# Optimization experiments

Hardware: AMD Instinct MI355X
Metric: run time of the kernel (lower is better)

## Reference

```python
import jax, jax.numpy as jnp
import numpy as np
import math

SAMPLE_RATIO = 0.25
K = 5
EPS = 1e-6

def _cells(loc_orig, H, W):
    # map normalized [-1,1] coords to nearest grid cell index, as in tcformer token2map/map2token
    loc = jnp.clip(loc_orig, -1.0, 1.0)
    px = jnp.clip(jnp.round(0.5 * (loc[..., 0] + 1.0) * W - 0.5).astype(jnp.int32), 0, W - 1)
    py = jnp.clip(jnp.round(0.5 * (loc[..., 1] + 1.0) * H - 0.5).astype(jnp.int32), 0, H - 1)
    return py * W + px  # [B, N0]

def token2map(x, loc_orig, idx_agg, H, W):
    B, N, C = x.shape
    N0 = loc_orig.shape[1]
    cell = _cells(loc_orig, H, W)
    seg = (cell + jnp.arange(B)[:, None] * (H * W)).reshape(-1)
    feat = x[jnp.arange(B)[:, None], idx_agg]  # [B, N0, C] token feature per original point
    sums = jax.ops.segment_sum(feat.reshape(-1, C), seg, num_segments=B * H * W)
    cnt = jax.ops.segment_sum(jnp.ones((B * N0,), x.dtype), seg, num_segments=B * H * W)
    x_map = sums / (cnt[:, None] + EPS)  # per-cell mean over points hitting the cell
    return x_map.reshape(B, H, W, C).transpose(0, 3, 1, 2)

def map2token(x_map, N, loc_orig, idx_agg, agg_weight):
    B, C, H, W = x_map.shape
    cell = _cells(loc_orig, H, W)
    val = x_map.reshape(B, C, H * W).transpose(0, 2, 1)  # [B, HW, C]
    vpt = val[jnp.arange(B)[:, None], cell]              # [B, N0, C] map value at each point
    seg = (idx_agg + jnp.arange(B)[:, None] * N).reshape(-1)
    w = agg_weight.reshape(-1)
    wsum = jax.ops.segment_sum(w, seg, num_segments=B * N) + EPS
    ssum = jax.ops.segment_sum(vpt.reshape(-1, C) * w[:, None], seg, num_segments=B * N)
    return (ssum / wsum[:, None]).reshape(B, N, C)  # agg_weight-weighted mean per token

def token_cluster_merge(x, Ns, idx_agg, weight, k):
    B, N, C = x.shape
    # DPC-KNN clustering (index computation; mirrors torch.no_grad block)
    sq = jnp.sum(x * x, -1)
    d2 = jnp.clip(sq[:, :, None] + sq[:, None, :] - 2.0 * jnp.einsum('bnc,bmc->bnm', x, x), 0.0, None)
    dist = jnp.sqrt(d2) / (C ** 0.5)
    dnear = -jax.lax.top_k(-dist, k)[0]                  # k smallest distances (incl. self)
    density = jnp.exp(-jnp.mean(dnear * dnear, -1))
    mask = density[:, None, :] > density[:, :, None]
    dmax = jnp.max(dist.reshape(B, -1), -1)[:, None, None]
    parent_dist = jnp.min(jnp.where(mask, dist, dmax), -1)  # dist to nearest higher-density token
    score = parent_dist * density
    index_down = jax.lax.top_k(score, Ns)[1]             # [B, Ns] cluster centers
    idx_cluster = jnp.argmin(dist[jnp.arange(B)[:, None], index_down], axis=1)  # [B, N]
    idx_cluster = idx_cluster.at[jnp.arange(B)[:, None], index_down].set(jnp.arange(Ns)[None, :])
    # weighted merge of tokens into clusters
    seg = (idx_cluster + jnp.arange(B)[:, None] * Ns).reshape(-1)
    w = weight.reshape(-1)
    allw = jax.ops.segment_sum(w, seg, num_segments=B * Ns) + EPS
    norm_w = (w / allw[seg]).reshape(B, N)
    x_merged = jax.ops.segment_sum((x * norm_w[:, :, None]).reshape(-1, C), seg, num_segments=B * Ns).reshape(B, Ns, C)
    idx_agg_down = idx_cluster[jnp.arange(B)[:, None], idx_agg]      # compose index maps
    weight_t = norm_w[jnp.arange(B)[:, None], idx_agg][..., None]    # [B, N0, 1]
    return x_merged, idx_agg_down, weight_t

def _forward(x, loc_orig, idx_agg, agg_weight, idx_k_loc, H, W, conv_w, conv_b, skip_w, ln_g, ln_b, conf_w, conf_b):
    B, N, C = x.shape
    x_map = token2map(x, loc_orig, idx_agg, H, W)
    x_map = jax.lax.conv_general_dilated(x_map, conv_w, (2, 2), ((1, 1), (1, 1))) + conv_b[None, :, None, None]
    x_tok = map2token(x_map, N, loc_orig, idx_agg, agg_weight) + jnp.einsum('bnc,oc->bno', x, skip_w)
    mu = jnp.mean(x_tok, -1, keepdims=True)
    var = jnp.mean((x_tok - mu) ** 2, -1, keepdims=True)
    x_tok = (x_tok - mu) / jnp.sqrt(var + 1e-5) * ln_g + ln_b
    conf = jnp.einsum('bnc,oc->bno', x_tok, conf_w) + conf_b
    weight = jnp.exp(conf)
    Ns = max(math.ceil(N * SAMPLE_RATIO), 1)
    x_down, idx_agg_down, weight_t = token_cluster_merge(x_tok, Ns, idx_agg, weight, K)
    agg_weight_down = agg_weight * weight_t
    agg_weight_down = agg_weight_down / jnp.max(agg_weight_down, axis=1, keepdims=True)
    # down_block is an injected submodule; treated as identity passthrough here
    return x_down, idx_agg_down, agg_weight_down

def setup_inputs():
    key = jax.random.key(0)
    ks = jax.random.split(key, 8)
    B, N, C, N0, Cout = 8, 256, 256, 16384, 512
    return {
        'x': jax.random.normal(ks[0], (B, N, C), jnp.float32),
        'loc_orig': jax.random.uniform(ks[1], (B, N0, 2), jnp.float32, -1.0, 1.0),
        'idx_agg': jax.random.randint(ks[2], (B, N0), 0, N),
        'agg_weight': jax.random.uniform(ks[3], (B, N0, 1), jnp.float32, 0.1, 1.0),
        'idx_k_loc': jax.random.randint(ks[4], (B, N0, K), 0, N0),
        'H': 64, 'W': 64,
        'conv_w': jax.random.normal(ks[5], (Cout, C, 3, 3), jnp.float32) * 0.02,
        'conv_b': jnp.zeros((Cout,), jnp.float32),
        'skip_w': jax.random.normal(ks[6], (Cout, C), jnp.float32) * 0.02,
        'ln_g': jnp.ones((Cout,), jnp.float32),
        'ln_b': jnp.zeros((Cout,), jnp.float32),
        'conf_w': jax.random.normal(ks[7], (1, Cout), jnp.float32) * 0.02,
        'conf_b': jnp.zeros((1,), jnp.float32),
    }

def reference(x, loc_orig, idx_agg, agg_weight, idx_k_loc, H, W, conv_w, conv_b, skip_w, ln_g, ln_b, conf_w, conf_b):
    return _forward(x, loc_orig, idx_agg, agg_weight, idx_k_loc, H, W, conv_w, conv_b, skip_w, ln_g, ln_b, conf_w, conf_b)
```

## Files before the change

### kernel.cpp

```cpp
#include <hip/hip_runtime.h>
#include <math.h>

typedef unsigned long long ull;
typedef __attribute__((ext_vector_type(8))) short short8v;
typedef __attribute__((ext_vector_type(4))) float float4v;

#define NB   8
#define NTOK 256
#define CIN  256
#define NP   16384
#define NCO  512
#define HW64 4096
#define OHW  1024
#define NS   64
#define EPS  1e-6f
#define KC   2304
#define NKC  72

#define AS1 __attribute__((address_space(1)))
#define AS3 __attribute__((address_space(3)))
__device__ __forceinline__ void gl_lds16(const unsigned short* g, unsigned short* l) {
    __builtin_amdgcn_global_load_lds((const AS1 unsigned*)g, (AS3 unsigned*)l, 16, 0, 0);
}

constexpr size_t OFF_SUMS = 0;
constexpr size_t OFF_CNT  = OFF_SUMS + (size_t)NB*HW64*CIN;
constexpr size_t OFF_AMAT = OFF_CNT  + (size_t)NB*HW64;
constexpr size_t OFF_ALLW = OFF_AMAT + (size_t)NB*NTOK*OHW;
constexpr size_t OFF_DMAX = OFF_ALLW + (size_t)NB*NS;
constexpr size_t OFF_MAXW = OFF_DMAX + NB;
constexpr size_t OFF_ZG   = OFF_MAXW + NB;
constexpr size_t ZERO_END = OFF_ZG + 8;
constexpr size_t OFF_WT   = ZERO_END;
constexpr size_t OFF_SKWT = OFF_WT   + (size_t)KC*NCO;
constexpr size_t OFF_Y    = OFF_SKWT + (size_t)CIN*NCO;
constexpr size_t OFF_C2   = OFF_Y    + (size_t)NB*OHW*NCO;
constexpr size_t OFF_WSUM = OFF_C2   + (size_t)NB*NTOK*NCO;
constexpr size_t OFF_XSKIP= OFF_WSUM + (size_t)NB*NTOK;
constexpr size_t OFF_XTOK = OFF_XSKIP+ (size_t)NB*NTOK*NCO;
constexpr size_t OFF_XPK  = OFF_XTOK + (size_t)NB*NTOK*NCO;
constexpr size_t OFF_WEXP = OFF_XPK  + (size_t)NB*NTOK*NCO;
constexpr size_t OFF_SQ   = OFF_WEXP + (size_t)NB*NTOK;
constexpr size_t OFF_DIST = OFF_SQ   + (size_t)NB*NTOK;
constexpr size_t OFF_DENS = OFF_DIST + (size_t)NB*NTOK*NTOK;
constexpr size_t OFF_SCORE= OFF_DENS + (size_t)NB*NTOK;
constexpr size_t OFF_IND  = OFF_SCORE+ (size_t)NB*NTOK;
constexpr size_t OFF_IDXCL= OFF_IND  + (size_t)NB*NS;
constexpr size_t OFF_NORMW= OFF_IDXCL+ (size_t)NB*NTOK;
constexpr size_t OFF_AWBUF= OFF_NORMW+ (size_t)NB*NTOK;
constexpr size_t OFF_XTPK = OFF_AWBUF+ (size_t)NB*NP;
constexpr size_t OFF_AMATP2= OFF_XTPK + (size_t)NB*CIN*NTOK;
constexpr size_t OFF_XTOKPK= OFF_Y;

__device__ __forceinline__ unsigned pack_hl(float x) {
    unsigned u = __float_as_uint(x);
    unsigned t = u + 0x7fffu + ((u >> 16) & 1u);
    unsigned hibits = t & 0xffff0000u;
    float lo = x - __uint_as_float(hibits);
    unsigned ul = __float_as_uint(lo);
    unsigned lt = ul + 0x7fffu + ((ul >> 16) & 1u);
    return hibits | (lt >> 16);
}
__device__ __forceinline__ unsigned hp2(unsigned w0, unsigned w1) {
    return __builtin_amdgcn_perm(w1, w0, 0x07060302u);
}
__device__ __forceinline__ unsigned lp2(unsigned w0, unsigned w1) {
    return __builtin_amdgcn_perm(w1, w0, 0x05040100u);
}

__global__ void hist(const float* __restrict__ loc, const int* __restrict__ idxagg,
                     const float* __restrict__ aggw,
                     int* __restrict__ cntmat, float* __restrict__ cnt,
                     float* __restrict__ amat) {
    int bp = blockIdx.x*256 + threadIdx.x;
    int b  = bp >> 14;
    float lx = loc[2*bp+0], ly = loc[2*bp+1];
    lx = fminf(fmaxf(lx, -1.f), 1.f);
    ly = fminf(fmaxf(ly, -1.f), 1.f);
    int px = (int)rintf((lx + 1.f)*32.f - 0.5f); px = min(max(px,0),63);
    int py = (int)rintf((ly + 1.f)*32.f - 0.5f); py = min(max(py,0),63);
    int cell = py*64 + px;
    int tok = idxagg[bp];
    atomicAdd(&cntmat[((size_t)(b*HW64 + cell))*NTOK + tok], 1);
    atomicAdd(&cnt[b*HW64 + cell], 1.0f);
    int qx = (int)rintf((lx + 1.f)*16.f - 0.5f); qx = min(max(qx,0),31);
    int qy = (int)rintf((ly + 1.f)*16.f - 0.5f); qy = min(max(qy,0),31);
    atomicAdd(&amat[((size_t)(b*NTOK + tok))*OHW + qy*32 + qx], aggw[bp]);
}

__global__ void cnt_pack(unsigned* __restrict__ m) {
    size_t i = (size_t)blockIdx.x*256 + threadIdx.x;
    int4 v = ((const int4*)m)[i];
    uint4 o;
    o.x = pack_hl((float)v.x); o.y = pack_hl((float)v.y);
    o.z = pack_hl((float)v.z); o.w = pack_hl((float)v.w);
    ((uint4*)m)[i] = o;
}

__global__ void xt_pack(const float* __restrict__ x, unsigned* __restrict__ xtpk) {
    int id = blockIdx.x*256 + threadIdx.x;
    int tok = id & 255, cin = (id >> 8) & 255, b = id >> 16;
    xtpk[id] = pack_hl(x[((size_t)(b*NTOK + tok))*CIN + cin]);
}

__global__ void wtrans(const float* __restrict__ convw, uint4* __restrict__ wtf) {
    int tid = blockIdx.x*256 + threadIdx.x;
    int lane = tid & 63;
    int r1 = tid >> 6;
    int h = r1 & 1;
    int r2 = r1 >> 1;
    int f = r2 & 3;
    int r3 = r2 >> 2;
    int kc = r3 % NKC, mt = r3 / NKC;
    int cout = mt*64 + f*16 + (lane & 15);
    int kb = kc*32 + (lane >> 4)*8;
    unsigned s[8];
    #pragma unroll
    for (int j = 0; j < 8; ++j) {
        int k = kb + j;
        int grp = k >> 8, cin = k & 255;
        unsigned w = pack_hl(convw[(size_t)cout*KC + cin*9 + grp]);
        s[j] = h ? (w & 0xffffu) : (w >> 16);
    }
    uint4 o;
    o.x = s[0] | (s[1]<<16); o.y = s[2] | (s[3]<<16);
    o.z = s[4] | (s[5]<<16); o.w = s[6] | (s[7]<<16);
    wtf[tid] = o;
}

__global__ void pack4(const float4* __restrict__ src, uint4* __restrict__ dst) {
    size_t i = (size_t)blockIdx.x*256 + threadIdx.x;
    float4 v = src[i];
    uint4 o;
    o.x = pack_hl(v.x); o.y = pack_hl(v.y); o.z = pack_hl(v.z); o.w = pack_hl(v.w);
    dst[i] = o;
}

__launch_bounds__(512)
__global__ void map_gemm(const unsigned* __restrict__ A, const unsigned* __restrict__ B,
                         const float* __restrict__ cnt, unsigned short* __restrict__ planes) {
    __shared__ __align__(16) unsigned short Ah[4096];
    __shared__ __align__(16) unsigned short Bh[8192], Bl[8192];
    int z = blockIdx.z, m0 = blockIdx.y*128;
    const unsigned* Ab = A + ((size_t)z*HW64 + m0)*NTOK;
    const unsigned* Bb = B + (size_t)z*CIN*NTOK;
    int t = threadIdx.x, lane = t & 63;
    int w = t >> 6;
    int wm = w >> 2, wn = w & 3;
    int l15 = lane & 15, l4 = lane >> 4;
    int rowA = t & 127, kgA = t >> 7;
    int rowB = t & 255, kgB0 = (t >> 8)*2;
    const unsigned* arow = Ab + (size_t)rowA*NTOK + kgA*8;
    const unsigned* brow = Bb + (size_t)rowB*NTOK + kgB0*8;
    int wbA = (rowA>>4)*512 + kgA*128 + (rowA&15)*8;
    int wbB = (rowB>>4)*512 + kgB0*128 + (rowB&15)*8;

    float4v acc[4][4] = {};
    uint4 ra0, ra1, rb[2][2];
    auto loadA = [&](int kc) {
        const unsigned* p = arow + kc*32;
        ra0 = *(const uint4*)p; ra1 = *(const uint4*)(p + 4);
    };
    auto loadB = [&](int kc) {
        #pragma unroll
        for (int s = 0; s < 2; ++s) {
            const unsigned* p = brow + kc*32 + s*8;
            rb[s][0] = *(const uint4*)p; rb[s][1] = *(const uint4*)(p + 4);
        }
    };
    loadA(0); loadB(0);

    for (int kc = 0; kc < 8; ++kc) {
        __syncthreads();
        uint4 h, l;
        h.x=hp2(ra0.x,ra0.y); h.y=hp2(ra0.z,ra0.w); h.z=hp2(ra1.x,ra1.y); h.w=hp2(ra1.z,ra1.w);
        *(uint4*)&Ah[wbA] = h;
        #pragma unroll
        for (int s = 0; s < 2; ++s) {
            uint4 u0 = rb[s][0], u1 = rb[s][1];
            h.x=hp2(u0.x,u0.y); h.y=hp2(u0.z,u0.w); h.z=hp2(u1.x,u1.y); h.w=hp2(u1.z,u1.w);
            l.x=lp2(u0.x,u0.y); l.y=lp2(u0.z,u0.w); l.z=lp2(u1.x,u1.y); l.w=lp2(u1.z,u1.w);
            *(uint4*)&Bh[wbB + s*128] = h; *(uint4*)&Bl[wbB + s*128] = l;
        }
        __syncthreads();
        if (kc < 7) { loadA(kc+1); loadB(kc+1); }

        short8v bh[4], bl[4];
        #pragma unroll
        for (int q = 0; q < 4; ++q) {
            int off = (wn*4 + q)*512 + l4*128 + l15*8;
            bh[q] = *(const short8v*)&Bh[off];
            bl[q] = *(const short8v*)&Bl[off];
        }
        #pragma unroll
        for (int p = 0; p < 4; ++p) {
            int off = (wm*4 + p)*512 + l4*128 + l15*8;
            short8v ah = *(const short8v*)&Ah[off];
            #pragma unroll
            for (int q = 0; q < 4; ++q) {
                acc[p][q] = __builtin_amdgcn_mfma_f32_16x16x32_bf16(ah, bh[q], acc[p][q], 0, 0, 0);
                acc[p][q] = __builtin_amdgcn_mfma_f32_16x16x32_bf16(ah, bl[q], acc[p][q], 0, 0, 0);
            }
        }
    }

    const float* cntb = cnt + (size_t)z*HW64;
    #pragma unroll
    for (int p = 0; p < 4; ++p) {
        int mb = m0 + wm*64 + p*16 + l4*4;
        #pragma unroll
        for (int q = 0; q < 4; ++q) {
            int n = wn*64 + q*16 + l15;
            #pragma unroll
            for (int r = 0; r < 4; ++r) {
                float v = acc[p][q][r] / (cntb[mb + r] + EPS);
                unsigned pk = pack_hl(v);
                size_t grow = (size_t)z*HW64 + mb + r;
                size_t base = (grow >> 7)*65536 + (grow & 127)*256 + n;
                planes[base]         = (unsigned short)(pk >> 16);
                planes[base + 32768] = (unsigned short)(pk & 0xffffu);
            }
        }
    }
}

__launch_bounds__(256)
__global__ void conv_gemm(const unsigned short* __restrict__ planes,
                          const uint4* __restrict__ wtf,
                          const float* __restrict__ convb,
                          const unsigned short* __restrict__ zg,
                          unsigned* __restrict__ ytp) {
    __shared__ __align__(16) unsigned short AH[2][4096], AL[2][4096];
    int n0 = blockIdx.x * 128;
    int mt = blockIdx.y;
    int m0 = mt * 64;
    int t = threadIdx.x;
    int lane = t & 63, w = t >> 6;
    int wm = w >> 1, wn = w & 1;
    int l15 = lane & 15, l4 = lane >> 4;
    int kg = l4;

    int bbS[2], oyS[2], oxS[2];
    #pragma unroll
    for (int s = 0; s < 2; ++s) {
        int pos = n0 + (w + s*4)*16 + l15;
        bbS[s] = pos >> 10; int rem = pos & 1023;
        oyS[s] = rem >> 5; oxS[s] = rem & 31;
    }
    auto stage = [&](int kc, int buf) {
        int grp = kc >> 3;
        int ky = grp/3, kx = grp - 3*ky;
        int kin = (kc & 7)*32 + kg*8;
        #pragma unroll
        for (int s = 0; s < 2; ++s) {
            int iy = 2*oyS[s] - 1 + ky, ix = 2*oxS[s] - 1 + kx;
            bool ok = ((unsigned)iy < 64u) && ((unsigned)ix < 64u);
            int srow = bbS[s]*HW64 + iy*64 + ix;
            const unsigned short* sp = planes + ((size_t)(srow >> 7))*65536 + (srow & 127)*256 + kin;
            const unsigned short* ph = ok ? sp : zg;
            const unsigned short* pl = ok ? sp + 32768 : zg;
            gl_lds16(ph, &AH[buf][(w + s*4)*512]);
            gl_lds16(pl, &AL[buf][(w + s*4)*512]);
        }
    };

    const uint4* wbase = wtf + ((size_t)(((mt*NKC)*4 + wn*2)*2))*64 + lane;
    float4v acc[4][2] = {};
    short8v bhc[2], blc[2], bhn[2], bln[2];
    #pragma unroll
    for (int q = 0; q < 2; ++q) {
        bhc[q] = *(const short8v*)(wbase + q*128);
        blc[q] = *(const short8v*)(wbase + q*128 + 64);
    }
    stage(0, 0);
    __syncthreads();
    int cur = 0;

    for (int kc = 0; kc < NKC; ++kc) {
        bool nl = (kc + 1 < NKC);
        if (nl) {
            stage(kc+1, cur ^ 1);
            const uint4* wb = wbase + (size_t)(kc+1)*512;
            #pragma unroll
            for (int q = 0; q < 2; ++q) {
                bhn[q] = *(const short8v*)(wb + q*128);
                bln[q] = *(const short8v*)(wb + q*128 + 64);
            }
        }
        #pragma unroll
        for (int p = 0; p < 4; ++p) {
            int off = (wm*4 + p)*512 + l4*128 + l15*8;
            short8v ah = *(const short8v*)&AH[cur][off];
            short8v al = *(const short8v*)&AL[cur][off];
            #pragma unroll
            for (int q = 0; q < 2; ++q) {
                acc[p][q] = __builtin_amdgcn_mfma_f32_16x16x32_bf16(ah, bhc[q], acc[p][q], 0, 0, 0);
                acc[p][q] = __builtin_amdgcn_mfma_f32_16x16x32_bf16(ah, blc[q], acc[p][q], 0, 0, 0);
                acc[p][q] = __builtin_amdgcn_mfma_f32_16x16x32_bf16(al, bhc[q], acc[p][q], 0, 0, 0);
            }
        }
        if (nl) {
            #pragma unroll
            for (int q = 0; q < 2; ++q) { bhc[q] = bhn[q]; blc[q] = bln[q]; }
        }
        __syncthreads();
        cur ^= 1;
    }

    int bbk = n0 >> 10;
    int pos0 = (n0 & 1023) + wm*64;
    #pragma unroll
    for (int p = 0; p < 4; ++p) {
        int posb = pos0 + p*16 + l4*4;
        #pragma unroll
        for (int q = 0; q < 2; ++q) {
            int col = m0 + wn*32 + q*16 + l15;
            float bv = convb[col];
            uint4 o;
            o.x = pack_hl(acc[p][q][0] + bv);
            o.y = pack_hl(acc[p][q][1] + bv);
            o.z = pack_hl(acc[p][q][2] + bv);
            o.w = pack_hl(acc[p][q][3] + bv);
            *(uint4*)&ytp[((size_t)(bbk*NCO + col))*OHW + posb] = o;
        }
    }
}

template<int MODE, int TM, int TN>
__launch_bounds__(256)
__global__ void gemm_pk(const unsigned* __restrict__ A, const unsigned* __restrict__ B,
                        float* __restrict__ C, int K, int N,
                        long sA, long sB, long sC,
                        const float* __restrict__ aux, unsigned* __restrict__ dmaxU) {
    constexpr int NA = TM/64, NBs = TN/64;
    constexpr int WSM = TM/64;
    constexpr int WSN = 4/WSM;
    constexpr int TWM = TM/WSM, TWN = TN/WSN;
    constexpr int P = TWM/16, Q = TWN/16;
    __shared__ __align__(16) unsigned short Ahi[TM*32], Alo[TM*32];
    __shared__ __align__(16) unsigned short Bhi[TN*32], Blo[TN*32];
    int z = blockIdx.z;
    const unsigned* Ab = A + (size_t)z*sA;
    const unsigned* Bb = B + (size_t)z*sB;
    float* Cb = C + (size_t)z*sC;
    int n0 = blockIdx.x*TN, m0 = blockIdx.y*TM;
    int t = threadIdx.x;
    int lane = t & 63, wid = t >> 6;
    int wm = (WSM==2) ? (wid >> 1) : 0;
    int wn = (WSM==2) ? (wid & 1)  : wid;
    int l15 = lane & 15, l4 = lane >> 4;

    int rowA = t & (TM-1), kgA = t / TM;
    int rowB = t & (TN-1), kgB = t / TN;
    const unsigned* arow = Ab + (size_t)(m0 + rowA)*K + kgA*8;
    const unsigned* brw  = Bb + (size_t)(n0 + rowB)*K + kgB*8;
    int wbA = (rowA>>4)*512 + kgA*128 + (rowA&15)*8;
    int wbB = (rowB>>4)*512 + kgB*128 + (rowB&15)*8;

    float4v acc[P][Q] = {};
    uint4 ra[NA][2], rb[NBs][2];
    auto loadA = [&](int kc) {
        #pragma unroll
        for (int s = 0; s < NA; ++s) {
            const unsigned* p = arow + (size_t)kc*32 + s*16;
            ra[s][0] = *(const uint4*)p; ra[s][1] = *(const uint4*)(p + 4);
        }
    };
    auto loadB = [&](int kc) {
        #pragma unroll
        for (int s = 0; s < NBs; ++s) {
            const unsigned* p = brw + (size_t)kc*32 + s*16;
            rb[s][0] = *(const uint4*)p; rb[s][1] = *(const uint4*)(p + 4);
        }
    };
    loadA(0); loadB(0);
    int nkc = K >> 5;

    for (int kc = 0; kc < nkc; ++kc) {
        __syncthreads();
        uint4 h, l;
        #pragma unroll
        for (int s = 0; s < NA; ++s) {
            uint4 u0 = ra[s][0], u1 = ra[s][1];
            h.x=hp2(u0.x,u0.y); h.y=hp2(u0.z,u0.w); h.z=hp2(u1.x,u1.y); h.w=hp2(u1.z,u1.w);
            l.x=lp2(u0.x,u0.y); l.y=lp2(u0.z,u0.w); l.z=lp2(u1.x,u1.y); l.w=lp2(u1.z,u1.w);
            *(uint4*)&Ahi[wbA + s*256] = h; *(uint4*)&Alo[wbA + s*256] = l;
        }
        #pragma unroll
        for (int s = 0; s < NBs; ++s) {
            uint4 u0 = rb[s][0], u1 = rb[s][1];
            h.x=hp2(u0.x,u0.y); h.y=hp2(u0.z,u0.w); h.z=hp2(u1.x,u1.y); h.w=hp2(u1.z,u1.w);
            l.x=lp2(u0.x,u0.y); l.y=lp2(u0.z,u0.w); l.z=lp2(u1.x,u1.y); l.w=lp2(u1.z,u1.w);
            *(uint4*)&Bhi[wbB + s*256] = h; *(uint4*)&Blo[wbB + s*256] = l;
        }
        __syncthreads();
        if (kc + 1 < nkc) { loadA(kc+1); loadB(kc+1); }

        short8v bh[Q], bl[Q];
        #pragma unroll
        for (int q = 0; q < Q; ++q) {
            int off = (wn*Q + q)*512 + l4*128 + l15*8;
            bh[q] = *(const short8v*)&Bhi[off];
            bl[q] = *(const short8v*)&Blo[off];
        }
        #pragma unroll
        for (int p = 0; p < P; ++p) {
            int off = (wm*P + p)*512 + l4*128 + l15*8;
            short8v ah = *(const short8v*)&Ahi[off];
            short8v al = *(const short8v*)&Alo[off];
            #pragma unroll
            for (int q = 0; q < Q; ++q) {
                acc[p][q] = __builtin_amdgcn_mfma_f32_16x16x32_bf16(ah, bh[q], acc[p][q], 0, 0, 0);
                acc[p][q] = __builtin_amdgcn_mfma_f32_16x16x32_bf16(ah, bl[q], acc[p][q], 0, 0, 0);
                acc[p][q] = __builtin_amdgcn_mfma_f32_16x16x32_bf16(al, bh[q], acc[p][q], 0, 0, 0);
            }
        }
    }

    if (MODE == 0) {
        #pragma unroll
        for (int p = 0; p < P; ++p) {
            int mb = m0 + wm*TWM + p*16 + l4*4;
            #pragma unroll
            for (int q = 0; q < Q; ++q) {
                int n = n0 + wn*TWN + q*16 + l15;
                #pragma unroll
                for (int r = 0; r < 4; ++r)
                    Cb[(size_t)(mb + r)*N + n] = acc[p][q][r];
            }
        }
    } else {
        const float inv = 1.0f / sqrtf(512.0f);
        const float* sqb = aux + (size_t)z*NTOK;
        float tmax = 0.f;
        #pragma unroll
        for (int p = 0; p < P; ++p) {
            int mb = m0 + wm*TWM + p*16 + l4*4;
            #pragma unroll
            for (int q = 0; q < Q; ++q) {
                int n = n0 + wn*TWN + q*16 + l15;
                float sn = sqb[n];
                #pragma unroll
                for (int r = 0; r < 4; ++r) {
                    float d2 = sqb[mb + r] + sn - 2.0f*acc[p][q][r];
                    float d = sqrtf(fmaxf(d2, 0.0f)) * inv;
                    Cb[(size_t)(mb + r)*N + n] = d;
                    tmax = fmaxf(tmax, d);
                }
            }
        }
        __shared__ float redm[4];
        #pragma unroll
        for (int off = 32; off; off >>= 1) tmax = fmaxf(tmax, __shfl_xor(tmax, off, 64));
        if (lane == 0) redm[wid] = tmax;
        __syncthreads();
        if (t == 0) {
            float m = fmaxf(fmaxf(redm[0], redm[1]), fmaxf(redm[2], redm[3]));
            atomicMax(dmaxU + z, __float_as_uint(m));
        }
    }
}

__global__ void wsum_rows(const float* __restrict__ amat, float* __restrict__ wsum) {
    int row = blockIdx.x*4 + (threadIdx.x >> 6);
    int lane = threadIdx.x & 63;
    const float* ar = amat + (size_t)row*OHW;
    float s = 0.f;
    #pragma unroll
    for (int r = 0; r < 16; ++r) s += ar[lane + 64*r];
    #pragma unroll
    for (int off = 32; off; off >>= 1) s += __shfl_xor(s, off, 64);
    if (lane == 0) wsum[row] = s;
}

__device__ __forceinline__ float block_sum256(float v, float* red) {
    #pragma unroll
    for (int off = 32; off; off >>= 1) v += __shfl_xor(v, off, 64);
    __syncthreads();
    if ((threadIdx.x & 63) == 0) red[threadIdx.x >> 6] = v;
    __syncthreads();
    return red[0] + red[1] + red[2] + red[3];
}

__global__ void ln_conf(const float* __restrict__ C2, const float* __restrict__ wsum,
                        const float* __restrict__ xskip, const float* __restrict__ g,
                        const float* __restrict__ be, const float* __restrict__ confw,
                        const float* __restrict__ confb, float* __restrict__ xtok,
                        unsigned* __restrict__ xtokpk,
                        float* __restrict__ wexp, float* __restrict__ sqv) {
    __shared__ float red[4];
    int row = blockIdx.x, t = threadIdx.x;
    float ws = wsum[row] + EPS;
    size_t base = (size_t)row*NCO;
    float v0 = C2[base + t]       / ws + xskip[base + t];
    float v1 = C2[base + t + 256] / ws + xskip[base + t + 256];
    float mu  = block_sum256(v0 + v1, red) / 512.0f;
    float d0 = v0 - mu, d1 = v1 - mu;
    float var = block_sum256(d0*d0 + d1*d1, red) / 512.0f;
    float sv = sqrtf(var + 1e-5f);
    float x0 = d0/sv * g[t]       + be[t];
    float x1 = d1/sv * g[t + 256] + be[t + 256];
    xtok[base + t] = x0;
    xtok[base + t + 256] = x1;
    xtokpk[base + t] = pack_hl(x0);
    xtokpk[base + t + 256] = pack_hl(x1);
    float cs = block_sum256(x0*confw[t] + x1*confw[t + 256], red);
    float qs = block_sum256(x0*x0 + x1*x1, red);
    if (t == 0) {
        wexp[row] = expf(cs + confb[0]);
        sqv[row]  = qs;
    }
}

__global__ void knn_dens(const float* __restrict__ dist, float* __restrict__ dens) {
    int row = blockIdx.x*4 + (threadIdx.x >> 6);
    int lane = threadIdx.x & 63;
    const float* dr = dist + (size_t)row*NTOK;
    float v0 = dr[lane], v1 = dr[lane+64], v2 = dr[lane+128], v3 = dr[lane+192];
    float acc = 0.f;
    #pragma unroll
    for (int it = 0; it < 5; ++it) {
        float lm = fminf(fminf(v0, v1), fminf(v2, v3));
        float gm = lm;
        #pragma unroll
        for (int off = 32; off; off >>= 1) gm = fminf(gm, __shfl_xor(gm, off, 64));
        acc += gm*gm;
        ull ball = __ballot(lm == gm);
        int first = __ffsll(ball) - 1;
        if (lane == first) {
            if      (v0 == gm) v0 = 1e30f;
            else if (v1 == gm) v1 = 1e30f;
            else if (v2 == gm) v2 = 1e30f;
            else               v3 = 1e30f;
        }
    }
    if (lane == 0) dens[row] = expf(-(acc/5.0f));
}

__global__ void parent_score(const float* __restrict__ dist, const float* __restrict__ dens,
                             const unsigned* __restrict__ dmaxU, float* __restrict__ score) {
    int row = blockIdx.x*4 + (threadIdx.x >> 6);
    int lane = threadIdx.x & 63;
    int b = row >> 8;
    float di = dens[row];
    float dm = __uint_as_float(dmaxU[b]);
    const float* dr = dist + (size_t)row*NTOK;
    const float* db = dens + (size_t)b*NTOK;
    float pd = dm;
    #pragma unroll
    for (int r = 0; r < 4; ++r) {
        int j = lane + 64*r;
        pd = fminf(pd, (db[j] > di) ? dr[j] : dm);
    }
    #pragma unroll
    for (int off = 32; off; off >>= 1) pd = fminf(pd, __shfl_xor(pd, off, 64));
    if (lane == 0) score[row] = pd * di;
}

__global__ void topk64(const float* __restrict__ score, int* __restrict__ ind) {
    int b = blockIdx.x, lane = threadIdx.x;
    const float* sb = score + b*NTOK;
    ull k0, k1, k2, k3;
    {
        unsigned i0 = lane, i1 = lane+64, i2 = lane+128, i3 = lane+192;
        k0 = ((ull)(__float_as_uint(sb[i0]) + 1u) << 32) | (unsigned)(4095 - i0);
        k1 = ((ull)(__float_as_uint(sb[i1]) + 1u) << 32) | (unsigned)(4095 - i1);
        k2 = ((ull)(__float_as_uint(sb[i2]) + 1u) << 32) | (unsigned)(4095 - i2);
        k3 = ((ull)(__float_as_uint(sb[i3]) + 1u) << 32) | (unsigned)(4095 - i3);
    }
    for (int it = 0; it < 64; ++it) {
        ull lm = k0;
        if (k1 > lm) lm = k1;
        if (k2 > lm) lm = k2;
        if (k3 > lm) lm = k3;
        ull gm = lm;
        #pragma unroll
        for (int off = 32; off; off >>= 1) {
            ull o = __shfl_xor(gm, off, 64);
            if (o > gm) gm = o;
        }
        if (lane == 0) ind[b*NS + it] = 4095 - (int)(gm & 0xffffffffull);
        if      (k0 == gm) k0 = 0;
        else if (k1 == gm) k1 = 0;
        else if (k2 == gm) k2 = 0;
        else if (k3 == gm) k3 = 0;
    }
}

__global__ void assign_k(const float* __restrict__ dist, const int* __restrict__ ind,
                         int* __restrict__ idxcl) {
    int row = blockIdx.x*4 + (threadIdx.x >> 6);
    int lane = threadIdx.x & 63;
    int b = row >> 8, i = row & 255;
    int center = ind[b*NS + lane];
    float d = dist[((size_t)(b*NTOK + center))*NTOK + i];
    ull key = ((ull)__float_as_uint(d) << 32) | (unsigned)lane;
    #pragma unroll
    for (int off = 32; off; off >>= 1) {
        ull o = __shfl_xor(key, off, 64);
        if (o < key) key = o;
    }
    if (lane == 0) idxcl[row] = (int)(key & 0xffffffffull);
}

__global__ void center_set(const int* __restrict__ ind, int* __restrict__ idxcl) {
    int id = threadIdx.x;
    int b = id >> 6, s = id & 63;
    idxcl[b*NTOK + ind[id]] = s;
}

__global__ void allw_acc(const int* __restrict__ idxcl, const float* __restrict__ wexp,
                         float* __restrict__ allw) {
    int b = blockIdx.x, i = threadIdx.x;
    atomicAdd(&allw[b*NS + idxcl[b*NTOK + i]], wexp[b*NTOK + i]);
}

__global__ void normw_k(const int* __restrict__ idxcl, const float* __restrict__ wexp,
                        const float* __restrict__ allw, float* __restrict__ normw) {
    int b = blockIdx.x, i = threadIdx.x;
    normw[b*NTOK + i] = wexp[b*NTOK + i] / (allw[b*NS + idxcl[b*NTOK + i]] + EPS);
}

__global__ void merge_k(const float* __restrict__ xtok, const int* __restrict__ idxcl,
                        const float* __restrict__ normw, float* __restrict__ xout) {
    int row = blockIdx.x, t = threadIdx.x;
    int b = row >> 8;
    int cl = idxcl[row];
    float nw = normw[row];
    float* o = xout + ((size_t)(b*NS + cl))*NCO;
    const float* xr = xtok + (size_t)row*NCO;
    atomicAdd(&o[t],       xr[t]       * nw);
    atomicAdd(&o[t + 256], xr[t + 256] * nw);
}

__global__ void out_idx_aw(const int* __restrict__ idxagg, const float* __restrict__ aggw,
                           const int* __restrict__ idxcl, const float* __restrict__ normw,
                           float* __restrict__ dout, float* __restrict__ awbuf,
                           unsigned* __restrict__ maxw) {
    __shared__ float red[4];
    int bp = blockIdx.x*256 + threadIdx.x;
    int b = bp >> 14;
    int tok = idxagg[bp];
    int cl = idxcl[b*NTOK + tok];
    dout[(size_t)NB*NS*NCO + bp] = (float)cl;
    float aw = aggw[bp] * normw[b*NTOK + tok];
    awbuf[bp] = aw;
    float m = aw;
    #pragma unroll
    for (int off = 32; off; off >>= 1) m = fmaxf(m, __shfl_xor(m, off, 64));
    if ((threadIdx.x & 63) == 0) red[threadIdx.x >> 6] = m;
    __syncthreads();
    if (threadIdx.x == 0) {
        float mm = fmaxf(fmaxf(red[0], red[1]), fmaxf(red[2], red[3]));
        atomicMax(&maxw[b], __float_as_uint(mm));
    }
}

__global__ void aw_final(const float* __restrict__ awbuf, const float* __restrict__ maxw,
                         float* __restrict__ dout) {
    int bp = blockIdx.x*256 + threadIdx.x;
    int b = bp >> 14;
    dout[(size_t)NB*NS*NCO + (size_t)NB*NP + bp] = awbuf[bp] / maxw[b];
}

extern "C" void kernel_launch(void* const* d_in, const int* in_sizes, int n_in,
                              void* d_out, int out_size, void* d_ws, size_t ws_size,
                              hipStream_t stream) {
    const float* x      = (const float*)d_in[0];
    const float* loc    = (const float*)d_in[1];
    const int*   idxagg = (const int*)  d_in[2];
    const float* aggw   = (const float*)d_in[3];
    const float* convw  = (const float*)d_in[7];
    const float* convb  = (const float*)d_in[8];
    const float* skipw  = (const float*)d_in[9];
    const float* lng    = (const float*)d_in[10];
    const float* lnb    = (const float*)d_in[11];
    const float* confw  = (const float*)d_in[12];
    const float* confb  = (const float*)d_in[13];

    float* ws = (float*)d_ws;
    float* dout = (float*)d_out;

    (void)hipMemsetAsync(ws, 0, ZERO_END*sizeof(float), stream);
    (void)hipMemsetAsync(dout, 0, (size_t)NB*NS*NCO*sizeof(float), stream);

    hist<<<dim3(NB*NP/256), 256, 0, stream>>>(loc, idxagg, aggw,
                                              (int*)(ws + OFF_SUMS), ws + OFF_CNT, ws + OFF_AMAT);
    cnt_pack<<<dim3(NB*HW64*CIN/1024), 256, 0, stream>>>((unsigned*)(ws + OFF_SUMS));
    xt_pack<<<dim3(NB*CIN*NTOK/256), 256, 0, stream>>>(x, (unsigned*)(ws + OFF_XTPK));
    wtrans<<<dim3(1152), 256, 0, stream>>>(convw, (uint4*)(ws + OFF_WT));
    pack4<<<dim3(CIN*NCO/1024), 256, 0, stream>>>((const float4*)skipw, (uint4*)(ws + OFF_SKWT));
    pack4<<<dim3(NB*NTOK*CIN/1024), 256, 0, stream>>>((const float4*)x, (uint4*)(ws + OFF_XPK));

    map_gemm<<<dim3(1, 32, 8), 512, 0, stream>>>((const unsigned*)(ws + OFF_SUMS),
                                                 (const unsigned*)(ws + OFF_XTPK),
                                                 ws + OFF_CNT,
                                                 (unsigned short*)(ws + OFF_SUMS));

    conv_gemm<<<dim3(64, 8), 256, 0, stream>>>((const unsigned short*)(ws + OFF_SUMS),
                                               (const uint4*)(ws + OFF_WT), convb,
                                               (const unsigned short*)(ws + OFF_ZG),
                                               (unsigned*)(ws + OFF_Y));

    wsum_rows<<<dim3(NB*NTOK/4), 256, 0, stream>>>(ws + OFF_AMAT, ws + OFF_WSUM);
    pack4<<<dim3(NB*NTOK*OHW/1024), 256, 0, stream>>>((const float4*)(ws + OFF_AMAT),
                                                      (uint4*)(ws + OFF_AMATP2));
    gemm_pk<0,64,64><<<dim3(8, 4, 8), 256, 0, stream>>>((const unsigned*)(ws + OFF_AMATP2),
                                                  (const unsigned*)(ws + OFF_Y),
                                                  ws + OFF_C2, OHW, NCO,
                                                  (long)NTOK*OHW, (long)NCO*OHW, (long)NTOK*NCO,
                                                  nullptr, nullptr);
    gemm_pk<0,64,64><<<dim3(8, 32, 1), 256, 0, stream>>>((const unsigned*)(ws + OFF_XPK),
                                                   (const unsigned*)(ws + OFF_SKWT),
                                                   ws + OFF_XSKIP, CIN, NCO, 0, 0, 0,
                                                   nullptr, nullptr);

    ln_conf<<<dim3(NB*NTOK), 256, 0, stream>>>(ws + OFF_C2, ws + OFF_WSUM, ws + OFF_XSKIP,
                                               lng, lnb, confw, confb,
                                               ws + OFF_XTOK, (unsigned*)(ws + OFF_XTOKPK),
                                               ws + OFF_WEXP, ws + OFF_SQ);

    gemm_pk<1,64,64><<<dim3(4, 4, 8), 256, 0, stream>>>((const unsigned*)(ws + OFF_XTOKPK),
                                                  (const unsigned*)(ws + OFF_XTOKPK),
                                                  ws + OFF_DIST, NCO, NTOK,
                                                  (long)NTOK*NCO, (long)NTOK*NCO, (long)NTOK*NTOK,
                                                  ws + OFF_SQ, (unsigned*)(ws + OFF_DMAX));

    knn_dens<<<dim3(NB*NTOK/4), 256, 0, stream>>>(ws + OFF_DIST, ws + OFF_DENS);
    parent_score<<<dim3(NB*NTOK/4), 256, 0, stream>>>(ws + OFF_DIST, ws + OFF_DENS,
                                                      (const unsigned*)(ws + OFF_DMAX), ws + OFF_SCORE);
    topk64<<<dim3(NB), 64, 0, stream>>>(ws + OFF_SCORE, (int*)(ws + OFF_IND));
    assign_k<<<dim3(NB*NTOK/4), 256, 0, stream>>>(ws + OFF_DIST, (const int*)(ws + OFF_IND),
                                                  (int*)(ws + OFF_IDXCL));
    center_set<<<dim3(1), 512, 0, stream>>>((const int*)(ws + OFF_IND), (int*)(ws + OFF_IDXCL));
    allw_acc<<<dim3(NB), 256, 0, stream>>>((const int*)(ws + OFF_IDXCL), ws + OFF_WEXP, ws + OFF_ALLW);
    normw_k<<<dim3(NB), 256, 0, stream>>>((const int*)(ws + OFF_IDXCL), ws + OFF_WEXP,
                                          ws + OFF_ALLW, ws + OFF_NORMW);
    merge_k<<<dim3(NB*NTOK), 256, 0, stream>>>(ws + OFF_XTOK, (const int*)(ws + OFF_IDXCL),
                                               ws + OFF_NORMW, dout);
    out_idx_aw<<<dim3(NB*NP/256), 256, 0, stream>>>(idxagg, aggw, (const int*)(ws + OFF_IDXCL),
                                                    ws + OFF_NORMW, dout, ws + OFF_AWBUF,
                                                    (unsigned*)(ws + OFF_MAXW));
    aw_final<<<dim3(NB*NP/256), 256, 0, stream>>>(ws + OFF_AWBUF, (const float*)(ws + OFF_MAXW), dout);
}
```

Before: 317.5 us.

## Split conv GEMM K across two blocks and revert to register-staged A loads

```diff
diff --git a/kernel.cpp b/kernel.cpp
--- a/kernel.cpp
+++ b/kernel.cpp
@@ -16,12 +16,7 @@
 #define EPS  1e-6f
 #define KC   2304
 #define NKC  72
-
-#define AS1 __attribute__((address_space(1)))
-#define AS3 __attribute__((address_space(3)))
-__device__ __forceinline__ void gl_lds16(const unsigned short* g, unsigned short* l) {
-    __builtin_amdgcn_global_load_lds((const AS1 unsigned*)g, (AS3 unsigned*)l, 16, 0, 0);
-}
+#define KSPL 36
 
 constexpr size_t OFF_SUMS = 0;
 constexpr size_t OFF_CNT  = OFF_SUMS + (size_t)NB*HW64*CIN;
@@ -29,8 +24,7 @@
 constexpr size_t OFF_ALLW = OFF_AMAT + (size_t)NB*NTOK*OHW;
 constexpr size_t OFF_DMAX = OFF_ALLW + (size_t)NB*NS;
 constexpr size_t OFF_MAXW = OFF_DMAX + NB;
-constexpr size_t OFF_ZG   = OFF_MAXW + NB;
-constexpr size_t ZERO_END = OFF_ZG + 8;
+constexpr size_t ZERO_END = OFF_MAXW + NB;
 constexpr size_t OFF_WT   = ZERO_END;
 constexpr size_t OFF_SKWT = OFF_WT   + (size_t)KC*NCO;
 constexpr size_t OFF_Y    = OFF_SKWT + (size_t)CIN*NCO;
@@ -50,6 +44,7 @@
 constexpr size_t OFF_AWBUF= OFF_NORMW+ (size_t)NB*NTOK;
 constexpr size_t OFF_XTPK = OFF_AWBUF+ (size_t)NB*NP;
 constexpr size_t OFF_AMATP2= OFF_XTPK + (size_t)NB*CIN*NTOK;
+constexpr size_t OFF_YPF1 = OFF_AMATP2+ (size_t)NB*NTOK*OHW;
 constexpr size_t OFF_XTOKPK= OFF_Y;
 
 __device__ __forceinline__ unsigned pack_hl(float x) {
@@ -138,7 +133,7 @@
 
 __launch_bounds__(512)
 __global__ void map_gemm(const unsigned* __restrict__ A, const unsigned* __restrict__ B,
-                         const float* __restrict__ cnt, unsigned short* __restrict__ planes) {
+                         const float* __restrict__ cnt, unsigned* __restrict__ xmapu) {
     __shared__ __align__(16) unsigned short Ah[4096];
     __shared__ __align__(16) unsigned short Bh[8192], Bl[8192];
     int z = blockIdx.z, m0 = blockIdx.y*128;
@@ -214,72 +209,76 @@
             #pragma unroll
             for (int r = 0; r < 4; ++r) {
                 float v = acc[p][q][r] / (cntb[mb + r] + EPS);
-                unsigned pk = pack_hl(v);
-                size_t grow = (size_t)z*HW64 + mb + r;
-                size_t base = (grow >> 7)*65536 + (grow & 127)*256 + n;
-                planes[base]         = (unsigned short)(pk >> 16);
-                planes[base + 32768] = (unsigned short)(pk & 0xffffu);
+                xmapu[((size_t)z*HW64 + mb + r)*CIN + n] = pack_hl(v);
             }
         }
     }
 }
 
 __launch_bounds__(256)
-__global__ void conv_gemm(const unsigned short* __restrict__ planes,
-                          const uint4* __restrict__ wtf,
-                          const float* __restrict__ convb,
-                          const unsigned short* __restrict__ zg,
-                          unsigned* __restrict__ ytp) {
-    __shared__ __align__(16) unsigned short AH[2][4096], AL[2][4096];
+__global__ void conv_gemm(const unsigned* __restrict__ xmap, const uint4* __restrict__ wtf,
+                          float* __restrict__ yp0, float* __restrict__ yp1) {
+    __shared__ __align__(16) unsigned short Ahi[2][4096], Alo[2][4096];
     int n0 = blockIdx.x * 128;
     int mt = blockIdx.y;
+    int zsp = blockIdx.z;
+    int kc0 = zsp * KSPL;
     int m0 = mt * 64;
     int t = threadIdx.x;
-    int lane = t & 63, w = t >> 6;
-    int wm = w >> 1, wn = w & 1;
+    int lane = t & 63, wid = t >> 6;
+    int wm = wid >> 1, wn = wid & 1;
     int l15 = lane & 15, l4 = lane >> 4;
-    int kg = l4;
-
-    int bbS[2], oyS[2], oxS[2];
-    #pragma unroll
-    for (int s = 0; s < 2; ++s) {
-        int pos = n0 + (w + s*4)*16 + l15;
-        bbS[s] = pos >> 10; int rem = pos & 1023;
-        oyS[s] = rem >> 5; oxS[s] = rem & 31;
-    }
-    auto stage = [&](int kc, int buf) {
+
+    int rowL = t & 127, kg = t >> 7;
+    int posG = n0 + rowL;
+    int bb = posG >> 10, rem = posG & 1023;
+    int oy = rem >> 5, ox = rem & 31;
+
+    int wbA0 = (rowL>>4)*512 + kg*128 + (rowL&15)*8;
+    int wbA1 = wbA0 + 256;
+
+    float4v acc[4][2] = {};
+    uint4 a00,a01,a10,a11;
+
+    auto loadA = [&](int kc) {
         int grp = kc >> 3;
         int ky = grp/3, kx = grp - 3*ky;
-        int kin = (kc & 7)*32 + kg*8;
-        #pragma unroll
-        for (int s = 0; s < 2; ++s) {
-            int iy = 2*oyS[s] - 1 + ky, ix = 2*oxS[s] - 1 + kx;
-            bool ok = ((unsigned)iy < 64u) && ((unsigned)ix < 64u);
-            int srow = bbS[s]*HW64 + iy*64 + ix;
-            const unsigned short* sp = planes + ((size_t)(srow >> 7))*65536 + (srow & 127)*256 + kin;
-            const unsigned short* ph = ok ? sp : zg;
-            const unsigned short* pl = ok ? sp + 32768 : zg;
-            gl_lds16(ph, &AH[buf][(w + s*4)*512]);
-            gl_lds16(pl, &AL[buf][(w + s*4)*512]);
+        int iy = 2*oy - 1 + ky, ix = 2*ox - 1 + kx;
+        if ((unsigned)iy < 64u && (unsigned)ix < 64u) {
+            const unsigned* ap = xmap + ((((size_t)bb*64 + iy)*64 + ix)*256 + (kc&7)*32 + kg*8);
+            a00 = *(const uint4*)ap;       a01 = *(const uint4*)(ap + 4);
+            a10 = *(const uint4*)(ap + 16); a11 = *(const uint4*)(ap + 20);
+        } else {
+            a00 = make_uint4(0,0,0,0); a01 = a00; a10 = a00; a11 = a00;
         }
     };
-
+    auto repackA = [&](int buf) {
+        uint4 h, l;
+        h.x=hp2(a00.x,a00.y); h.y=hp2(a00.z,a00.w); h.z=hp2(a01.x,a01.y); h.w=hp2(a01.z,a01.w);
+        l.x=lp2(a00.x,a00.y); l.y=lp2(a00.z,a00.w); l.z=lp2(a01.x,a01.y); l.w=lp2(a01.z,a01.w);
+        *(uint4*)&Ahi[buf][wbA0] = h; *(uint4*)&Alo[buf][wbA0] = l;
+        h.x=hp2(a10.x,a10.y); h.y=hp2(a10.z,a10.w); h.z=hp2(a11.x,a11.y); h.w=hp2(a11.z,a11.w);
+        l.x=lp2(a10.x,a10.y); l.y=lp2(a10.z,a10.w); l.z=lp2(a11.x,a11.y); l.w=lp2(a11.z,a11.w);
+        *(uint4*)&Ahi[buf][wbA1] = h; *(uint4*)&Alo[buf][wbA1] = l;
+    };
     const uint4* wbase = wtf + ((size_t)(((mt*NKC)*4 + wn*2)*2))*64 + lane;
-    float4v acc[4][2] = {};
+
     short8v bhc[2], blc[2], bhn[2], bln[2];
     #pragma unroll
     for (int q = 0; q < 2; ++q) {
-        bhc[q] = *(const short8v*)(wbase + q*128);
-        blc[q] = *(const short8v*)(wbase + q*128 + 64);
-    }
-    stage(0, 0);
+        bhc[q] = *(const short8v*)(wbase + (size_t)kc0*512 + q*128);
+        blc[q] = *(const short8v*)(wbase + (size_t)kc0*512 + q*128 + 64);
+    }
+    loadA(kc0);
+    repackA(0);
     __syncthreads();
     int cur = 0;
 
-    for (int kc = 0; kc < NKC; ++kc) {
-        bool nl = (kc + 1 < NKC);
+    for (int it = 0; it < KSPL; ++it) {
+        int kc = kc0 + it;
+        bool nl = (it + 1 < KSPL);
         if (nl) {
-            stage(kc+1, cur ^ 1);
+            loadA(kc+1);
             const uint4* wb = wbase + (size_t)(kc+1)*512;
             #pragma unroll
             for (int q = 0; q < 2; ++q) {
@@ -290,8 +289,8 @@
         #pragma unroll
         for (int p = 0; p < 4; ++p) {
             int off = (wm*4 + p)*512 + l4*128 + l15*8;
-            short8v ah = *(const short8v*)&AH[cur][off];
-            short8v al = *(const short8v*)&AL[cur][off];
+            short8v ah = *(const short8v*)&Ahi[cur][off];
+            short8v al = *(const short8v*)&Alo[cur][off];
             #pragma unroll
             for (int q = 0; q < 2; ++q) {
                 acc[p][q] = __builtin_amdgcn_mfma_f32_16x16x32_bf16(ah, bhc[q], acc[p][q], 0, 0, 0);
@@ -300,6 +299,7 @@
             }
         }
         if (nl) {
+            repackA(cur ^ 1);
             #pragma unroll
             for (int q = 0; q < 2; ++q) { bhc[q] = bhn[q]; blc[q] = bln[q]; }
         }
@@ -307,6 +307,7 @@
         cur ^= 1;
     }
 
+    float* yp = (zsp == 0) ? yp0 : yp1;
     int bbk = n0 >> 10;
     int pos0 = (n0 & 1023) + wm*64;
     #pragma unroll
@@ -315,15 +316,23 @@
         #pragma unroll
         for (int q = 0; q < 2; ++q) {
             int col = m0 + wn*32 + q*16 + l15;
-            float bv = convb[col];
-            uint4 o;
-            o.x = pack_hl(acc[p][q][0] + bv);
-            o.y = pack_hl(acc[p][q][1] + bv);
-            o.z = pack_hl(acc[p][q][2] + bv);
-            o.w = pack_hl(acc[p][q][3] + bv);
-            *(uint4*)&ytp[((size_t)(bbk*NCO + col))*OHW + posb] = o;
-        }
-    }
+            *(float4v*)&yp[((size_t)(bbk*NCO + col))*OHW + posb] = acc[p][q];
+        }
+    }
+}
+
+__global__ void y_reduce(const float4* __restrict__ p0, const float4* __restrict__ p1,
+                         const float* __restrict__ convb, uint4* __restrict__ out) {
+    size_t i = (size_t)blockIdx.x*256 + threadIdx.x;
+    int col = (int)((i >> 8) & 511);
+    float bv = convb[col];
+    float4 a = p0[i], b = p1[i];
+    uint4 o;
+    o.x = pack_hl(a.x + b.x + bv);
+    o.y = pack_hl(a.y + b.y + bv);
+    o.z = pack_hl(a.z + b.z + bv);
+    o.w = pack_hl(a.w + b.w + bv);
+    out[i] = o;
 }
 
 template<int MODE, int TM, int TN>
@@ -695,12 +704,14 @@
     map_gemm<<<dim3(1, 32, 8), 512, 0, stream>>>((const unsigned*)(ws + OFF_SUMS),
                                                  (const unsigned*)(ws + OFF_XTPK),
                                                  ws + OFF_CNT,
-                                                 (unsigned short*)(ws + OFF_SUMS));
-
-    conv_gemm<<<dim3(64, 8), 256, 0, stream>>>((const unsigned short*)(ws + OFF_SUMS),
-                                               (const uint4*)(ws + OFF_WT), convb,
-                                               (const unsigned short*)(ws + OFF_ZG),
-                                               (unsigned*)(ws + OFF_Y));
+                                                 (unsigned*)(ws + OFF_SUMS));
+
+    conv_gemm<<<dim3(64, 8, 2), 256, 0, stream>>>((const unsigned*)(ws + OFF_SUMS),
+                                                  (const uint4*)(ws + OFF_WT),
+                                                  ws + OFF_Y, ws + OFF_YPF1);
+    y_reduce<<<dim3(4096), 256, 0, stream>>>((const float4*)(ws + OFF_Y),
+                                             (const float4*)(ws + OFF_YPF1),
+                                             convb, (uint4*)(ws + OFF_Y));
 
     wsum_rows<<<dim3(NB*NTOK/4), 256, 0, stream>>>(ws + OFF_AMAT, ws + OFF_WSUM);
     pack4<<<dim3(NB*NTOK*OHW/1024), 256, 0, stream>>>((const float4*)(ws + OFF_AMAT),
```

Result: no change. 315.7 us (-0.6%).
